# Performance work log

Hardware: AMD Instinct MI355X
Metric: run time of the kernel (lower is better)

Reference implementation:

```python
import jax, jax.numpy as jnp
import numpy as np

B, N, DIM, H, DH = 8, 1024, 512, 8, 64
INNER = H * DH
SCALE = DH ** -0.5
EPS = 1e-12  # F.normalize eps


def setup_inputs() -> dict:
    key = jax.random.key(0)
    k1, k2, k3, k4, k5 = jax.random.split(key, 5)
    x = jax.random.normal(k1, (B, N, DIM), dtype=jnp.float32)
    spd = jax.random.normal(k2, (B, 1, N, N), dtype=jnp.float32)
    # per-head binomial keep mask (one realized draw of the original loop), guaranteed nonzero
    a = np.random.RandomState(0).binomial(1, 0.9, size=H)
    if a.sum() == 0:
        a[0] = 1
    head_mask = jnp.asarray(a, dtype=jnp.float32)
    W_qkv = jax.random.normal(k3, (DIM, 3 * INNER), dtype=jnp.float32) * (DIM ** -0.5)
    W_out = jax.random.normal(k4, (INNER, DIM), dtype=jnp.float32) * (INNER ** -0.5)
    b_out = jax.random.normal(k5, (DIM,), dtype=jnp.float32) * 0.01
    return {"x": x, "spd": spd, "head_mask": head_mask,
            "W_qkv": W_qkv, "W_out": W_out, "b_out": b_out}


def reference(x, spd, head_mask, W_qkv, W_out, b_out):
    b, n, _ = x.shape
    qkv = x @ W_qkv                                   # [b, n, 3*inner]
    q, k, v = jnp.split(qkv, 3, axis=-1)
    split_heads = lambda t: t.reshape(b, n, H, DH).transpose(0, 2, 1, 3)  # b h n d
    q, k, v = split_heads(q), split_heads(k), split_heads(v)

    dots = jnp.einsum('bhnd,bhmd->bhnm', q, k) * SCALE        # [b,h,n,n]
    prod = dots * spd                                         # broadcast spd over heads
    prod_norm = jnp.sqrt(jnp.sum(prod * prod, axis=-1, keepdims=True))
    dots_norm = jnp.sqrt(jnp.sum(dots * dots, axis=-1, keepdims=True))
    bias = prod / jnp.maximum(prod_norm, EPS) * dots_norm     # F.normalize(prod)*||dots||
    attn = jax.nn.softmax(dots + bias, axis=-1)

    # head dropout mask with rescale: attn * mask * H / sum(mask)
    scale_m = head_mask * (H / jnp.sum(head_mask))
    attn = attn * scale_m[None, :, None, None]

    out = jnp.einsum('bhnm,bhmd->bhnd', attn, v)              # [b,h,n,d]
    out = out.transpose(0, 2, 1, 3).reshape(b, n, INNER)      # b n (h d)
    return out @ W_out + b_out
```

## Files before the change

kernel.cpp:

```cpp
#include <hip/hip_runtime.h>
#include <hip/hip_bf16.h>

typedef __attribute__((ext_vector_type(8))) short short8;
typedef __attribute__((ext_vector_type(4))) short s16x4;
typedef __attribute__((ext_vector_type(4))) float f32x4;

typedef const __attribute__((address_space(1))) unsigned* gp1;
typedef __attribute__((address_space(3))) unsigned* lp3;

__device__ inline short f2bf(float f) {
    union { float f; unsigned u; } v; v.f = f;
    unsigned r = v.u + 0x7fffu + ((v.u >> 16) & 1u);
    return (short)(r >> 16);
}

__global__ __launch_bounds__(256) void cvt_bf16(
    const float* __restrict__ src, short* __restrict__ dst, int n4)
{
    int i = blockIdx.x * 256 + threadIdx.x;
    if (i < n4) {
        float4 v = ((const float4*)src)[i];
        s16x4 o = { f2bf(v.x), f2bf(v.y), f2bf(v.z), f2bf(v.w) };
        ((s16x4*)dst)[i] = o;
    }
}

__global__ __launch_bounds__(256) void tr_w(
    const float* __restrict__ src, short* __restrict__ dst, int K, int N)
{
    __shared__ float t[64][65];
    const int k0 = blockIdx.x * 64, n0 = blockIdx.y * 64;
    const int r = threadIdx.x >> 4, c4 = (threadIdx.x & 15) * 4;
#pragma unroll
    for (int j = 0; j < 4; j++) {
        float4 v = *(const float4*)(src + (size_t)(k0 + r + 16 * j) * N + n0 + c4);
        t[r + 16 * j][c4 + 0] = v.x; t[r + 16 * j][c4 + 1] = v.y;
        t[r + 16 * j][c4 + 2] = v.z; t[r + 16 * j][c4 + 3] = v.w;
    }
    __syncthreads();
#pragma unroll
    for (int j = 0; j < 4; j++) {
        const int n = r + 16 * j;
        s16x4 o = { f2bf(t[c4 + 0][n]), f2bf(t[c4 + 1][n]),
                    f2bf(t[c4 + 2][n]), f2bf(t[c4 + 3][n]) };
        *(s16x4*)(dst + (size_t)(n0 + n) * K + k0 + c4) = o;
    }
}

__global__ __launch_bounds__(256) void qkv_gemm(
    const short* __restrict__ A, const short* __restrict__ BT,
    short* __restrict__ q, short* __restrict__ k, short* __restrict__ vt)
{
    __shared__ short sA[128][32];
    __shared__ short sB[128][32];

    const int tid  = threadIdx.x;
    const int wv   = tid >> 6, lane = tid & 63;
    const int quad = lane >> 4, l16 = lane & 15;
    const int wr = wv >> 1, wc = wv & 1;
    const int m0 = blockIdx.x * 128, n0 = blockIdx.y * 128;

    f32x4 acc[4][4];
#pragma unroll
    for (int i = 0; i < 4; i++)
#pragma unroll
        for (int j = 0; j < 4; j++) acc[i][j] = (f32x4){0.f, 0.f, 0.f, 0.f};

    const short* a_src = A  + (size_t)(m0 + wv * 32 + (lane >> 2)) * 512 + (lane & 3) * 8;
    const short* b_src = BT + (size_t)(n0 + wv * 32 + (lane >> 2)) * 512 + (lane & 3) * 8;
    char* a_dst = (char*)sA + wv * 2048;
    char* b_dst = (char*)sB + wv * 2048;

    for (int ks = 0; ks < 16; ks++) {
        __syncthreads();
        const short* ap = a_src + ks * 32;
        const short* bp = b_src + ks * 32;
        __builtin_amdgcn_global_load_lds((gp1)(ap),            (lp3)(a_dst),        16, 0, 0);
        __builtin_amdgcn_global_load_lds((gp1)(ap + 16 * 512), (lp3)(a_dst + 1024), 16, 0, 0);
        __builtin_amdgcn_global_load_lds((gp1)(bp),            (lp3)(b_dst),        16, 0, 0);
        __builtin_amdgcn_global_load_lds((gp1)(bp + 16 * 512), (lp3)(b_dst + 1024), 16, 0, 0);
        __syncthreads();

        short8 af[4], bf[4];
#pragma unroll
        for (int f = 0; f < 4; f++) {
            af[f] = *(const short8*)&sA[wr * 64 + f * 16 + l16][quad * 8];
            bf[f] = *(const short8*)&sB[wc * 64 + f * 16 + l16][quad * 8];
        }
#pragma unroll
        for (int fm = 0; fm < 4; fm++)
#pragma unroll
            for (int fn = 0; fn < 4; fn++)
                acc[fm][fn] = __builtin_amdgcn_mfma_f32_16x16x32_bf16(
                    af[fm], bf[fn], acc[fm][fn], 0, 0, 0);
    }

    const int sec = n0 >> 9;
#pragma unroll
    for (int fn = 0; fn < 4; fn++) {
        const int gc = n0 + wc * 64 + fn * 16 + l16;
        const int cc = gc & 511;
        const int h = cc >> 6, d = cc & 63;
#pragma unroll
        for (int fm = 0; fm < 4; fm++)
#pragma unroll
            for (int i = 0; i < 4; i++) {
                const int gm = m0 + wr * 64 + fm * 16 + quad * 4 + i;
                const int b = gm >> 10, n = gm & 1023;
                const int bh = b * 8 + h;
                if (sec == 0)      q[((size_t)(bh * 1024 + n)) * 64 + d] = f2bf(acc[fm][fn][i] * 0.125f);
                else if (sec == 1) k[((size_t)(bh * 1024 + n)) * 64 + d] = f2bf(acc[fm][fn][i]);
                else               vt[((size_t)(bh * 64 + d)) * 1024 + n] = f2bf(acc[fm][fn][i]);
            }
    }
}

__global__ __launch_bounds__(256, 4) void attn_k(
    const short* __restrict__ q, const short* __restrict__ kk,
    const short* __restrict__ vt, const float* __restrict__ spd,
    const float* __restrict__ hm, short* __restrict__ o)
{
    __shared__ short sK[64][72];
    __shared__ short sV[64][72];
    __shared__ short sP[4][16][72];
    __shared__ float sred[4][16];

    const int tid  = threadIdx.x;
    const int wv   = tid >> 6, lane = tid & 63;
    const int quad = lane >> 4, l16 = lane & 15;
    const int qt = blockIdx.x, bh = blockIdx.y;
    const int b = bh >> 3, h = bh & 7;
    const int q0 = qt * 64;

    const short* qb = q + ((size_t)bh * 1024 + q0 + wv * 16 + l16) * 64;
    short8 aq0 = *(const short8*)(qb + quad * 8);
    short8 aq1 = *(const short8*)(qb + 32 + quad * 8);

    const int sr = tid & 31, sc = (tid >> 5) * 8;
    const short* ksrc = kk + (size_t)bh * 65536 + (size_t)sr * 64 + sc;
    const short* vsrc = vt + (size_t)bh * 65536 + (size_t)sr * 1024 + sc;
    const float* sp   = spd + ((size_t)b * 1024 + q0 + wv * 16 + l16) * 1024 + quad * 4;

    float dn = 0.f, pn = 0.f;
    short8 k0 = *(const short8*)(ksrc);
    short8 k1 = *(const short8*)(ksrc + 2048);
    float4 sv0 = *(const float4*)(sp +  0);
    float4 sv1 = *(const float4*)(sp + 16);
    float4 sv2 = *(const float4*)(sp + 32);
    float4 sv3 = *(const float4*)(sp + 48);

    for (int c = 0; c < 16; ++c) {
        __syncthreads();
        *(short8*)&sK[sr][sc]      = k0;
        *(short8*)&sK[sr + 32][sc] = k1;
        __syncthreads();
        float4 svc0 = sv0, svc1 = sv1, svc2 = sv2, svc3 = sv3;
        if (c < 15) {
            k0 = *(const short8*)(ksrc + (c + 1) * 4096);
            k1 = *(const short8*)(ksrc + (c + 1) * 4096 + 2048);
            sv0 = *(const float4*)(sp + (c + 1) * 64 +  0);
            sv1 = *(const float4*)(sp + (c + 1) * 64 + 16);
            sv2 = *(const float4*)(sp + (c + 1) * 64 + 32);
            sv3 = *(const float4*)(sp + (c + 1) * 64 + 48);
        }
        f32x4 a[4];
#pragma unroll
        for (int t = 0; t < 4; t++) {
            a[t] = (f32x4){0.f, 0.f, 0.f, 0.f};
            a[t] = __builtin_amdgcn_mfma_f32_16x16x32_bf16(
                *(const short8*)&sK[t * 16 + l16][quad * 8], aq0, a[t], 0, 0, 0);
            a[t] = __builtin_amdgcn_mfma_f32_16x16x32_bf16(
                *(const short8*)&sK[t * 16 + l16][32 + quad * 8], aq1, a[t], 0, 0, 0);
        }
        const float4 svv[4] = {svc0, svc1, svc2, svc3};
#pragma unroll
        for (int t = 0; t < 4; t++)
#pragma unroll
            for (int i = 0; i < 4; i++) {
                float s  = a[t][i];
                float sv = ((const float*)&svv[t])[i];
                float ps = s * sv;
                dn = fmaf(s, s, dn);
                pn = fmaf(ps, ps, pn);
            }
    }
    dn += __shfl_xor(dn, 16, 64); dn += __shfl_xor(dn, 32, 64);
    pn += __shfl_xor(pn, 16, 64); pn += __shfl_xor(pn, 32, 64);
    const float ratio = sqrtf(dn) / fmaxf(sqrtf(pn), 1e-12f);

    float m_r = -1e30f, ls = 0.f;
    f32x4 O[4];
#pragma unroll
    for (int dt = 0; dt < 4; dt++) O[dt] = (f32x4){0.f, 0.f, 0.f, 0.f};

    k0 = *(const short8*)(ksrc);
    k1 = *(const short8*)(ksrc + 2048);
    short8 v0 = *(const short8*)(vsrc);
    short8 v1 = *(const short8*)(vsrc + 32768);

    for (int c = 0; c < 16; ++c) {
        __syncthreads();
        *(short8*)&sK[sr][sc]      = k0;
        *(short8*)&sK[sr + 32][sc] = k1;
        *(short8*)&sV[sr][sc]      = v0;
        *(short8*)&sV[sr + 32][sc] = v1;
        __syncthreads();
        float4 svc0 = *(const float4*)(sp + c * 64 +  0);
        float4 svc1 = *(const float4*)(sp + c * 64 + 16);
        float4 svc2 = *(const float4*)(sp + c * 64 + 32);
        float4 svc3 = *(const float4*)(sp + c * 64 + 48);
        if (c < 15) {
            k0 = *(const short8*)(ksrc + (c + 1) * 4096);
            k1 = *(const short8*)(ksrc + (c + 1) * 4096 + 2048);
            v0 = *(const short8*)(vsrc + (c + 1) * 64);
            v1 = *(const short8*)(vsrc + (c + 1) * 64 + 32768);
        }
        f32x4 a[4];
#pragma unroll
        for (int t = 0; t < 4; t++) {
            a[t] = (f32x4){0.f, 0.f, 0.f, 0.f};
            a[t] = __builtin_amdgcn_mfma_f32_16x16x32_bf16(
                *(const short8*)&sK[t * 16 + l16][quad * 8], aq0, a[t], 0, 0, 0);
            a[t] = __builtin_amdgcn_mfma_f32_16x16x32_bf16(
                *(const short8*)&sK[t * 16 + l16][32 + quad * 8], aq1, a[t], 0, 0, 0);
        }
        const float4 svv[4] = {svc0, svc1, svc2, svc3};
        float mx = -1e30f;
#pragma unroll
        for (int t = 0; t < 4; t++)
#pragma unroll
            for (int i = 0; i < 4; i++) {
                float s  = a[t][i];
                float sv = ((const float*)&svv[t])[i];
                float l  = s * fmaf(sv, ratio, 1.0f);
                a[t][i] = l;
                mx = fmaxf(mx, l);
            }
        mx = fmaxf(mx, __shfl_xor(mx, 16, 64));
        mx = fmaxf(mx, __shfl_xor(mx, 32, 64));
        const float m_new = fmaxf(m_r, mx);
        const float fo = __expf(m_r - m_new);
        m_r = m_new;
        ls *= fo;
        float fov[4];
#pragma unroll
        for (int i = 0; i < 4; i++) fov[i] = __shfl(fo, quad * 4 + i, 16);
#pragma unroll
        for (int dt = 0; dt < 4; dt++) {
            O[dt][0] *= fov[0]; O[dt][1] *= fov[1];
            O[dt][2] *= fov[2]; O[dt][3] *= fov[3];
        }
#pragma unroll
        for (int t = 0; t < 4; t++) {
            float p0 = __expf(a[t][0] - m_r);
            float p1 = __expf(a[t][1] - m_r);
            float p2 = __expf(a[t][2] - m_r);
            float p3 = __expf(a[t][3] - m_r);
            ls += (p0 + p1) + (p2 + p3);
            s16x4 pk = { f2bf(p0), f2bf(p1), f2bf(p2), f2bf(p3) };
            *(s16x4*)&sP[wv][l16][t * 16 + quad * 4] = pk;
        }
#pragma unroll
        for (int kc = 0; kc < 2; kc++) {
            short8 pa = *(const short8*)&sP[wv][l16][kc * 32 + quad * 8];
#pragma unroll
            for (int dt = 0; dt < 4; dt++) {
                short8 vf = *(const short8*)&sV[dt * 16 + l16][kc * 32 + quad * 8];
                O[dt] = __builtin_amdgcn_mfma_f32_16x16x32_bf16(pa, vf, O[dt], 0, 0, 0);
            }
        }
    }
    ls += __shfl_xor(ls, 16, 64); ls += __shfl_xor(ls, 32, 64);
    const float hsum = hm[0] + hm[1] + hm[2] + hm[3] + hm[4] + hm[5] + hm[6] + hm[7];
    const float rinv = hm[h] * 8.0f / (hsum * ls);
    if (quad == 0) sred[wv][l16] = rinv;
    __syncthreads();
    float rv[4];
#pragma unroll
    for (int i = 0; i < 4; i++) rv[i] = sred[wv][quad * 4 + i];
#pragma unroll
    for (int dt = 0; dt < 4; dt++)
#pragma unroll
        for (int i = 0; i < 4; i++)
            o[((size_t)(b * 1024 + q0 + wv * 16 + quad * 4 + i)) * 512 + h * 64 + dt * 16 + l16]
                = f2bf(O[dt][i] * rv[i]);
}

__global__ __launch_bounds__(256) void out_gemm(
    const short* __restrict__ A, const short* __restrict__ BT,
    const float* __restrict__ bias, float* __restrict__ out)
{
    __shared__ short sA[128][32];
    __shared__ short sB[128][32];

    const int tid  = threadIdx.x;
    const int wv   = tid >> 6, lane = tid & 63;
    const int quad = lane >> 4, l16 = lane & 15;
    const int wr = wv >> 1, wc = wv & 1;
    const int m0 = blockIdx.x * 128, n0 = blockIdx.y * 128;

    f32x4 acc[4][4];
#pragma unroll
    for (int i = 0; i < 4; i++)
#pragma unroll
        for (int j = 0; j < 4; j++) acc[i][j] = (f32x4){0.f, 0.f, 0.f, 0.f};

    const short* a_src = A  + (size_t)(m0 + wv * 32 + (lane >> 2)) * 512 + (lane & 3) * 8;
    const short* b_src = BT + (size_t)(n0 + wv * 32 + (lane >> 2)) * 512 + (lane & 3) * 8;
    char* a_dst = (char*)sA + wv * 2048;
    char* b_dst = (char*)sB + wv * 2048;

    for (int ks = 0; ks < 16; ks++) {
        __syncthreads();
        const short* ap = a_src + ks * 32;
        const short* bp = b_src + ks * 32;
        __builtin_amdgcn_global_load_lds((gp1)(ap),            (lp3)(a_dst),        16, 0, 0);
        __builtin_amdgcn_global_load_lds((gp1)(ap + 16 * 512), (lp3)(a_dst + 1024), 16, 0, 0);
        __builtin_amdgcn_global_load_lds((gp1)(bp),            (lp3)(b_dst),        16, 0, 0);
        __builtin_amdgcn_global_load_lds((gp1)(bp + 16 * 512), (lp3)(b_dst + 1024), 16, 0, 0);
        __syncthreads();

        short8 af[4], bf[4];
#pragma unroll
        for (int f = 0; f < 4; f++) {
            af[f] = *(const short8*)&sA[wr * 64 + f * 16 + l16][quad * 8];
            bf[f] = *(const short8*)&sB[wc * 64 + f * 16 + l16][quad * 8];
        }
#pragma unroll
        for (int fm = 0; fm < 4; fm++)
#pragma unroll
            for (int fn = 0; fn < 4; fn++)
                acc[fm][fn] = __builtin_amdgcn_mfma_f32_16x16x32_bf16(
                    af[fm], bf[fn], acc[fm][fn], 0, 0, 0);
    }

#pragma unroll
    for (int fn = 0; fn < 4; fn++) {
        const int gc = n0 + wc * 64 + fn * 16 + l16;
        const float bv = bias[gc];
#pragma unroll
        for (int fm = 0; fm < 4; fm++)
#pragma unroll
            for (int i = 0; i < 4; i++) {
                const int gm = m0 + wr * 64 + fm * 16 + quad * 4 + i;
                out[(size_t)gm * 512 + gc] = acc[fm][fn][i] + bv;
            }
    }
}

extern "C" void kernel_launch(void* const* d_in, const int* in_sizes, int n_in,
                              void* d_out, int out_size, void* d_ws, size_t ws_size,
                              hipStream_t stream) {
    const float* x    = (const float*)d_in[0];
    const float* spd  = (const float*)d_in[1];
    const float* hm   = (const float*)d_in[2];
    const float* Wqkv = (const float*)d_in[3];
    const float* Wout = (const float*)d_in[4];
    const float* bout = (const float*)d_in[5];
    float* out = (float*)d_out;

    char* ws = (char*)d_ws;
    short* qw  = (short*)(ws);
    short* kw  = (short*)(ws + ((size_t)8  << 20));
    short* vtw = (short*)(ws + ((size_t)16 << 20));
    short* ow  = (short*)(ws + ((size_t)24 << 20));
    short* xb  = (short*)(ws + ((size_t)32 << 20));
    short* wqT = (short*)(ws + ((size_t)40 << 20));
    short* woT = (short*)(ws + ((size_t)42 << 20));

    cvt_bf16<<<4096, 256, 0, stream>>>(x, xb, 8192 * 512 / 4);
    tr_w    <<<dim3(8, 24), 256, 0, stream>>>(Wqkv, wqT, 512, 1536);
    tr_w    <<<dim3(8, 8),  256, 0, stream>>>(Wout, woT, 512, 512);

    qkv_gemm<<<dim3(64, 12), 256, 0, stream>>>(xb, wqT, qw, kw, vtw);
    attn_k  <<<dim3(16, 64), 256, 0, stream>>>(qw, kw, vtw, spd, hm, ow);
    out_gemm<<<dim3(64, 4),  256, 0, stream>>>(ow, woT, bout, out);
}
```

Measured before the change: 250.2 us.

## Convert spd to fp16, transpose V separately, double-buffer K in norm pass

Adds a pre-pass that converts the spd matrix to fp16 so the attention kernel's two passes over spd read half the bytes. The QKV GEMM now writes V in row layout instead of a strided scatter, and a new tr_v kernel transposes it through shared memory. The first (norm) pass of attention double-buffers the K tile in LDS to drop one barrier per iteration. The trade-off is two extra kernel launches, an extra full read and write of spd, and fp16 rounding of spd values.

```diff
diff --git a/kernel.cpp b/kernel.cpp
--- a/kernel.cpp
+++ b/kernel.cpp
@@ -4,6 +4,7 @@
 typedef __attribute__((ext_vector_type(8))) short short8;
 typedef __attribute__((ext_vector_type(4))) short s16x4;
 typedef __attribute__((ext_vector_type(4))) float f32x4;
+typedef __attribute__((ext_vector_type(4))) _Float16 h4;
 
 typedef const __attribute__((address_space(1))) unsigned* gp1;
 typedef __attribute__((address_space(3))) unsigned* lp3;
@@ -25,6 +26,17 @@
     }
 }
 
+__global__ __launch_bounds__(256) void cvt_spd(
+    const float* __restrict__ src, _Float16* __restrict__ dst, int n4)
+{
+    int i = blockIdx.x * 256 + threadIdx.x;
+    if (i < n4) {
+        float4 v = ((const float4*)src)[i];
+        h4 o = { (_Float16)v.x, (_Float16)v.y, (_Float16)v.z, (_Float16)v.w };
+        ((h4*)dst)[i] = o;
+    }
+}
+
 __global__ __launch_bounds__(256) void tr_w(
     const float* __restrict__ src, short* __restrict__ dst, int K, int N)
 {
@@ -47,9 +59,34 @@
     }
 }
 
+__global__ __launch_bounds__(256) void tr_v(
+    const short* __restrict__ src, short* __restrict__ dst)
+{
+    __shared__ short t[64][72];
+    const int bh = blockIdx.y, n0 = blockIdx.x * 64;
+    const int r = threadIdx.x >> 3;
+    const int c8 = (threadIdx.x & 7) * 8;
+    const short* s = src + ((size_t)bh * 1024 + n0) * 64;
+#pragma unroll
+    for (int j = 0; j < 2; j++) {
+        short8 v = *(const short8*)(s + (size_t)(r + 32 * j) * 64 + c8);
+        *(short8*)&t[r + 32 * j][c8] = v;
+    }
+    __syncthreads();
+    short* dptr = dst + (size_t)bh * 65536;
+#pragma unroll
+    for (int j = 0; j < 2; j++) {
+        const int d = r + 32 * j;
+        s16x4 lo = { t[c8 + 0][d], t[c8 + 1][d], t[c8 + 2][d], t[c8 + 3][d] };
+        s16x4 hi = { t[c8 + 4][d], t[c8 + 5][d], t[c8 + 6][d], t[c8 + 7][d] };
+        *(s16x4*)(dptr + (size_t)d * 1024 + n0 + c8)     = lo;
+        *(s16x4*)(dptr + (size_t)d * 1024 + n0 + c8 + 4) = hi;
+    }
+}
+
 __global__ __launch_bounds__(256) void qkv_gemm(
     const short* __restrict__ A, const short* __restrict__ BT,
-    short* __restrict__ q, short* __restrict__ k, short* __restrict__ vt)
+    short* __restrict__ q, short* __restrict__ k, short* __restrict__ vw)
 {
     __shared__ short sA[128][32];
     __shared__ short sB[128][32];
@@ -108,19 +145,19 @@
                 const int gm = m0 + wr * 64 + fm * 16 + quad * 4 + i;
                 const int b = gm >> 10, n = gm & 1023;
                 const int bh = b * 8 + h;
-                if (sec == 0)      q[((size_t)(bh * 1024 + n)) * 64 + d] = f2bf(acc[fm][fn][i] * 0.125f);
-                else if (sec == 1) k[((size_t)(bh * 1024 + n)) * 64 + d] = f2bf(acc[fm][fn][i]);
-                else               vt[((size_t)(bh * 64 + d)) * 1024 + n] = f2bf(acc[fm][fn][i]);
+                if (sec == 0)      q[((size_t)(bh * 1024 + n)) * 64 + d]  = f2bf(acc[fm][fn][i] * 0.125f);
+                else if (sec == 1) k[((size_t)(bh * 1024 + n)) * 64 + d]  = f2bf(acc[fm][fn][i]);
+                else               vw[((size_t)(bh * 1024 + n)) * 64 + d] = f2bf(acc[fm][fn][i]);
             }
     }
 }
 
 __global__ __launch_bounds__(256, 4) void attn_k(
     const short* __restrict__ q, const short* __restrict__ kk,
-    const short* __restrict__ vt, const float* __restrict__ spd,
+    const short* __restrict__ vt, const _Float16* __restrict__ spdh,
     const float* __restrict__ hm, short* __restrict__ o)
 {
-    __shared__ short sK[64][72];
+    __shared__ short sK[2][64][72];
     __shared__ short sV[64][72];
     __shared__ short sP[4][16][72];
     __shared__ float sred[4][16];
@@ -139,50 +176,60 @@
     const int sr = tid & 31, sc = (tid >> 5) * 8;
     const short* ksrc = kk + (size_t)bh * 65536 + (size_t)sr * 64 + sc;
     const short* vsrc = vt + (size_t)bh * 65536 + (size_t)sr * 1024 + sc;
-    const float* sp   = spd + ((size_t)b * 1024 + q0 + wv * 16 + l16) * 1024 + quad * 4;
+    const _Float16* sph = spdh + ((size_t)b * 1024 + q0 + wv * 16 + l16) * 1024 + quad * 4;
 
     float dn = 0.f, pn = 0.f;
-    short8 k0 = *(const short8*)(ksrc);
-    short8 k1 = *(const short8*)(ksrc + 2048);
-    float4 sv0 = *(const float4*)(sp +  0);
-    float4 sv1 = *(const float4*)(sp + 16);
-    float4 sv2 = *(const float4*)(sp + 32);
-    float4 sv3 = *(const float4*)(sp + 48);
+    short8 ka0 = *(const short8*)(ksrc);
+    short8 ka1 = *(const short8*)(ksrc + 2048);
+    short8 kb0 = *(const short8*)(ksrc + 4096);
+    short8 kb1 = *(const short8*)(ksrc + 4096 + 2048);
+    h4 sv0 = *(const h4*)(sph +  0);
+    h4 sv1 = *(const h4*)(sph + 16);
+    h4 sv2 = *(const h4*)(sph + 32);
+    h4 sv3 = *(const h4*)(sph + 48);
+    *(short8*)&sK[0][sr][sc]      = ka0;
+    *(short8*)&sK[0][sr + 32][sc] = ka1;
+    __syncthreads();
 
     for (int c = 0; c < 16; ++c) {
-        __syncthreads();
-        *(short8*)&sK[sr][sc]      = k0;
-        *(short8*)&sK[sr + 32][sc] = k1;
-        __syncthreads();
-        float4 svc0 = sv0, svc1 = sv1, svc2 = sv2, svc3 = sv3;
+        const int cur = c & 1;
         if (c < 15) {
-            k0 = *(const short8*)(ksrc + (c + 1) * 4096);
-            k1 = *(const short8*)(ksrc + (c + 1) * 4096 + 2048);
-            sv0 = *(const float4*)(sp + (c + 1) * 64 +  0);
-            sv1 = *(const float4*)(sp + (c + 1) * 64 + 16);
-            sv2 = *(const float4*)(sp + (c + 1) * 64 + 32);
-            sv3 = *(const float4*)(sp + (c + 1) * 64 + 48);
+            if (c & 1) { *(short8*)&sK[cur ^ 1][sr][sc] = ka0; *(short8*)&sK[cur ^ 1][sr + 32][sc] = ka1; }
+            else       { *(short8*)&sK[cur ^ 1][sr][sc] = kb0; *(short8*)&sK[cur ^ 1][sr + 32][sc] = kb1; }
+        }
+        if (c < 14) {
+            if (c & 1) { kb0 = *(const short8*)(ksrc + (c + 2) * 4096);
+                         kb1 = *(const short8*)(ksrc + (c + 2) * 4096 + 2048); }
+            else       { ka0 = *(const short8*)(ksrc + (c + 2) * 4096);
+                         ka1 = *(const short8*)(ksrc + (c + 2) * 4096 + 2048); }
+        }
+        h4 svc[4] = { sv0, sv1, sv2, sv3 };
+        if (c < 15) {
+            sv0 = *(const h4*)(sph + (c + 1) * 64 +  0);
+            sv1 = *(const h4*)(sph + (c + 1) * 64 + 16);
+            sv2 = *(const h4*)(sph + (c + 1) * 64 + 32);
+            sv3 = *(const h4*)(sph + (c + 1) * 64 + 48);
         }
         f32x4 a[4];
 #pragma unroll
         for (int t = 0; t < 4; t++) {
             a[t] = (f32x4){0.f, 0.f, 0.f, 0.f};
             a[t] = __builtin_amdgcn_mfma_f32_16x16x32_bf16(
-                *(const short8*)&sK[t * 16 + l16][quad * 8], aq0, a[t], 0, 0, 0);
+                *(const short8*)&sK[cur][t * 16 + l16][quad * 8], aq0, a[t], 0, 0, 0);
             a[t] = __builtin_amdgcn_mfma_f32_16x16x32_bf16(
-                *(const short8*)&sK[t * 16 + l16][32 + quad * 8], aq1, a[t], 0, 0, 0);
-        }
-        const float4 svv[4] = {svc0, svc1, svc2, svc3};
+                *(const short8*)&sK[cur][t * 16 + l16][32 + quad * 8], aq1, a[t], 0, 0, 0);
+        }
 #pragma unroll
         for (int t = 0; t < 4; t++)
 #pragma unroll
             for (int i = 0; i < 4; i++) {
                 float s  = a[t][i];
-                float sv = ((const float*)&svv[t])[i];
+                float sv = (float)svc[t][i];
                 float ps = s * sv;
                 dn = fmaf(s, s, dn);
                 pn = fmaf(ps, ps, pn);
             }
+        __syncthreads();
     }
     dn += __shfl_xor(dn, 16, 64); dn += __shfl_xor(dn, 32, 64);
     pn += __shfl_xor(pn, 16, 64); pn += __shfl_xor(pn, 32, 64);
@@ -193,22 +240,23 @@
 #pragma unroll
     for (int dt = 0; dt < 4; dt++) O[dt] = (f32x4){0.f, 0.f, 0.f, 0.f};
 
-    k0 = *(const short8*)(ksrc);
-    k1 = *(const short8*)(ksrc + 2048);
+    short8 k0 = *(const short8*)(ksrc);
+    short8 k1 = *(const short8*)(ksrc + 2048);
     short8 v0 = *(const short8*)(vsrc);
     short8 v1 = *(const short8*)(vsrc + 32768);
 
     for (int c = 0; c < 16; ++c) {
         __syncthreads();
-        *(short8*)&sK[sr][sc]      = k0;
-        *(short8*)&sK[sr + 32][sc] = k1;
+        *(short8*)&sK[0][sr][sc]      = k0;
+        *(short8*)&sK[0][sr + 32][sc] = k1;
         *(short8*)&sV[sr][sc]      = v0;
         *(short8*)&sV[sr + 32][sc] = v1;
         __syncthreads();
-        float4 svc0 = *(const float4*)(sp + c * 64 +  0);
-        float4 svc1 = *(const float4*)(sp + c * 64 + 16);
-        float4 svc2 = *(const float4*)(sp + c * 64 + 32);
-        float4 svc3 = *(const float4*)(sp + c * 64 + 48);
+        h4 svh[4];
+        svh[0] = *(const h4*)(sph + c * 64 +  0);
+        svh[1] = *(const h4*)(sph + c * 64 + 16);
+        svh[2] = *(const h4*)(sph + c * 64 + 32);
+        svh[3] = *(const h4*)(sph + c * 64 + 48);
         if (c < 15) {
             k0 = *(const short8*)(ksrc + (c + 1) * 4096);
             k1 = *(const short8*)(ksrc + (c + 1) * 4096 + 2048);
@@ -220,18 +268,17 @@
         for (int t = 0; t < 4; t++) {
             a[t] = (f32x4){0.f, 0.f, 0.f, 0.f};
             a[t] = __builtin_amdgcn_mfma_f32_16x16x32_bf16(
-                *(const short8*)&sK[t * 16 + l16][quad * 8], aq0, a[t], 0, 0, 0);
+                *(const short8*)&sK[0][t * 16 + l16][quad * 8], aq0, a[t], 0, 0, 0);
             a[t] = __builtin_amdgcn_mfma_f32_16x16x32_bf16(
-                *(const short8*)&sK[t * 16 + l16][32 + quad * 8], aq1, a[t], 0, 0, 0);
-        }
-        const float4 svv[4] = {svc0, svc1, svc2, svc3};
+                *(const short8*)&sK[0][t * 16 + l16][32 + quad * 8], aq1, a[t], 0, 0, 0);
+        }
         float mx = -1e30f;
 #pragma unroll
         for (int t = 0; t < 4; t++)
 #pragma unroll
             for (int i = 0; i < 4; i++) {
                 float s  = a[t][i];
-                float sv = ((const float*)&svv[t])[i];
+                float sv = (float)svh[t][i];
                 float l  = s * fmaf(sv, ratio, 1.0f);
                 a[t][i] = l;
                 mx = fmaxf(mx, l);
@@ -364,15 +411,19 @@
     short* kw  = (short*)(ws + ((size_t)8  << 20));
     short* vtw = (short*)(ws + ((size_t)16 << 20));
     short* ow  = (short*)(ws + ((size_t)24 << 20));
+    short* vw  = (short*)(ws + ((size_t)24 << 20));
     short* xb  = (short*)(ws + ((size_t)32 << 20));
     short* wqT = (short*)(ws + ((size_t)40 << 20));
     short* woT = (short*)(ws + ((size_t)42 << 20));
+    _Float16* spdh = (_Float16*)(ws + ((size_t)43 << 20));
 
     cvt_bf16<<<4096, 256, 0, stream>>>(x, xb, 8192 * 512 / 4);
+    cvt_spd <<<8192, 256, 0, stream>>>(spd, spdh, 8 * 1024 * 1024 / 4);
     tr_w    <<<dim3(8, 24), 256, 0, stream>>>(Wqkv, wqT, 512, 1536);
     tr_w    <<<dim3(8, 8),  256, 0, stream>>>(Wout, woT, 512, 512);
 
-    qkv_gemm<<<dim3(64, 12), 256, 0, stream>>>(xb, wqT, qw, kw, vtw);
-    attn_k  <<<dim3(16, 64), 256, 0, stream>>>(qw, kw, vtw, spd, hm, ow);
+    qkv_gemm<<<dim3(64, 12), 256, 0, stream>>>(xb, wqT, qw, kw, vw);
+    tr_v    <<<dim3(16, 64), 256, 0, stream>>>(vw, vtw);
+    attn_k  <<<dim3(16, 64), 256, 0, stream>>>(qw, kw, vtw, spdh, hm, ow);
     out_gemm<<<dim3(64, 4),  256, 0, stream>>>(ow, woT, bout, out);
 }
```

Measured after the change: 264.5 us. +5.7%, slower.
